# Optimization experiments

Measured on AMD Instinct MI355X. Metric: run time of the kernel, lower is better.

Reference implementation:

```python
import jax, jax.numpy as jnp
import numpy as np

B, L, S, H, E = 2, 2048, 2048, 16, 64


def setup_inputs() -> dict:
    key = jax.random.key(0)
    kq, kk, kv = jax.random.split(key, 3)
    queries = jax.random.normal(kq, (B, L, H, E), dtype=jnp.float32)
    keys = jax.random.normal(kk, (B, S, H, E), dtype=jnp.float32)
    values = jax.random.normal(kv, (B, S, H, E), dtype=jnp.float32)
    attn_mask = jnp.ones((B, 1, L, S), dtype=jnp.float32)  # >0.5 means attend
    return {"queries": queries, "keys": keys, "values": values, "attn_mask": attn_mask}


def reference(queries, keys, values, attn_mask):
    # queries: [B,L,H,E], keys/values: [B,S,H,E], attn_mask broadcastable to [B,H,L,S]
    E_ = queries.shape[-1]
    scale = 1.0 / np.sqrt(E_).astype(np.float32)
    scores = jnp.einsum('blhe,bshe->bhls', queries, keys)  # [B,H,L,S]
    large_negative = jnp.float32(-1e9)
    scores = scores + jnp.where(attn_mask > 0.5, jnp.float32(0.0), large_negative)
    A = jax.nn.softmax(scale * scores, axis=-1)  # dropout p=0.0 -> identity
    V = jnp.einsum('bhls,bshd->bhld', A, values)  # [B,H,L,D]
    return V
```

## Files before the change

### kernel.cpp

```cpp
#include <hip/hip_runtime.h>

typedef float f32x4 __attribute__((ext_vector_type(4)));
typedef short s16x8 __attribute__((ext_vector_type(8)));
typedef int   i32x4 __attribute__((ext_vector_type(4)));
typedef int   i32x2 __attribute__((ext_vector_type(2)));

namespace {
constexpr int B_ = 2, L_ = 2048, S_ = 2048, H_ = 16, E_ = 64;
constexpr int MBLK = 128;
constexpr int NT = 64;
constexpr int NTILES = S_ / NT;
constexpr int KPAD = 72;

#define SCALE2f 0.1803368801111204f
#define MBIAS2f -1.8033688e8f

__device__ __forceinline__ unsigned pk2(float a, float b) {
  unsigned ua = __builtin_bit_cast(unsigned, a) + 0x8000u;
  unsigned ub = __builtin_bit_cast(unsigned, b) + 0x8000u;
  return __builtin_amdgcn_perm(ub, ua, 0x07060302u);
}
__device__ __forceinline__ short f2bs(float x) {
  return (short)((__builtin_bit_cast(unsigned, x) + 0x8000u) >> 16);
}
}

extern "C" __global__ __launch_bounds__(256)
void maskpack_kernel(const float* __restrict__ Mg, unsigned long long* __restrict__ Wb) {
  const int w    = (int)((blockIdx.x * 256 + threadIdx.x) >> 6);
  const int lane = threadIdx.x & 63;
  const float* src = Mg + (size_t)w * 4096 + lane;
  unsigned long long* dst = Wb + (size_t)w * 64;
#pragma unroll 4
  for (int j = 0; j < 64; ++j) {
    const float m = src[j * 64];
    const unsigned long long bits = __ballot(m > 0.5f);
    if (lane == 0) dst[j] = bits;
  }
}

extern "C" __global__ __launch_bounds__(256, 2)
void fattn_kernel(const float* __restrict__ Qg, const float* __restrict__ Kg,
                  const float* __restrict__ Vg, const unsigned long long* __restrict__ Wb,
                  float* __restrict__ Og) {
  __shared__ __align__(16) short Ks[2][NT][KPAD];
  __shared__ __align__(16) short Vt[2][E_][KPAD];
  __shared__ __align__(16) short Ps[4][32][KPAD];

  const int tid  = threadIdx.x;
  const int wv   = tid >> 6;
  const int lane = tid & 63;
  const int qd   = lane >> 4;
  const int cl   = lane & 15;

  const int bid = blockIdx.x;
  const int qb  = bid >> 5;
  const int bh  = bid & 31;
  const int h   = bh & (H_ - 1);
  const int b   = bh >> 4;

  const int l0 = qb * MBLK + wv * 32;

  s16x8 qf[2][2];
#pragma unroll
  for (int mt = 0; mt < 2; ++mt) {
    const float* qp = Qg + ((((size_t)b * L_ + (l0 + mt * 16 + cl)) * H_ + h) << 6);
#pragma unroll
    for (int kb = 0; kb < 2; ++kb) {
      const int e0 = qd * 8 + kb * 32;
      f32x4 x = *(const f32x4*)(qp + e0);
      f32x4 y = *(const f32x4*)(qp + e0 + 4);
      i32x4 w = {(int)pk2(x[0], x[1]), (int)pk2(x[2], x[3]),
                 (int)pk2(y[0], y[1]), (int)pk2(y[2], y[3])};
      qf[mt][kb] = __builtin_bit_cast(s16x8, w);
    }
  }

  const int krow = tid >> 2;
  const int kc0  = (tid & 3) << 4;
  const int vs   = tid & 63;
  const int ve0  = (tid >> 6) << 4;

  const float* kptr = Kg + ((((size_t)b * S_ + krow) * H_ + h) << 6) + kc0;
  const float* vptr = Vg + ((((size_t)b * S_ + vs) * H_ + h) << 6) + ve0;
  const size_t tstep = (size_t)NT * H_ * E_;

  const unsigned long long* wbp[2];
  wbp[0] = Wb + (((size_t)b * L_ + (l0 + cl)) << 5);
  wbp[1] = Wb + (((size_t)b * L_ + (l0 + 16 + cl)) << 5);

  f32x4 kr[4], vr[4];
#pragma unroll
  for (int i = 0; i < 4; ++i) {
    kr[i] = *(const f32x4*)(kptr + i * 4);
    vr[i] = *(const f32x4*)(vptr + i * 4);
  }

  const f32x4 zero4 = {0.f, 0.f, 0.f, 0.f};
  f32x4 acc[2][4];
#pragma unroll
  for (int mt = 0; mt < 2; ++mt)
#pragma unroll
    for (int et = 0; et < 4; ++et) acc[mt][et] = zero4;
  f32x4 rs4[2] = {zero4, zero4};

  {
    i32x4 w0 = {(int)pk2(kr[0][0], kr[0][1]), (int)pk2(kr[0][2], kr[0][3]),
                (int)pk2(kr[1][0], kr[1][1]), (int)pk2(kr[1][2], kr[1][3])};
    i32x4 w1 = {(int)pk2(kr[2][0], kr[2][1]), (int)pk2(kr[2][2], kr[2][3]),
                (int)pk2(kr[3][0], kr[3][1]), (int)pk2(kr[3][2], kr[3][3])};
    *(i32x4*)&Ks[0][krow][kc0]     = w0;
    *(i32x4*)&Ks[0][krow][kc0 + 8] = w1;
#pragma unroll
    for (int j = 0; j < 4; ++j)
#pragma unroll
      for (int c = 0; c < 4; ++c) Vt[0][ve0 + j * 4 + c][vs] = f2bs(vr[j][c]);
  }
#pragma unroll
  for (int i = 0; i < 4; ++i) {
    kr[i] = *(const f32x4*)(kptr + tstep + i * 4);
    vr[i] = *(const f32x4*)(vptr + tstep + i * 4);
  }
  unsigned long long mwcur[2] = {wbp[0][0], wbp[1][0]};

  for (int t = 0; t < NTILES; ++t) {
    const int cb = t & 1;
    __syncthreads();

    unsigned long long mwnext[2];
    if (t + 1 < NTILES) {
      mwnext[0] = wbp[0][t + 1];
      mwnext[1] = wbp[1][t + 1];
    }

    f32x4 sc[4][2];
#pragma unroll
    for (int nt = 0; nt < 4; ++nt) {
      const s16x8 a0 = *(const s16x8*)&Ks[cb][nt * 16 + cl][qd * 8];
      const s16x8 a1 = *(const s16x8*)&Ks[cb][nt * 16 + cl][qd * 8 + 32];
#pragma unroll
      for (int mt = 0; mt < 2; ++mt) {
        f32x4 c = zero4;
        c = __builtin_amdgcn_mfma_f32_16x16x32_bf16(a0, qf[mt][0], c, 0, 0, 0);
        c = __builtin_amdgcn_mfma_f32_16x16x32_bf16(a1, qf[mt][1], c, 0, 0, 0);
        sc[nt][mt] = c;
      }
    }

#pragma unroll
    for (int mt = 0; mt < 2; ++mt) {
      const unsigned lo = (unsigned)mwcur[mt];
      const unsigned hi = (unsigned)(mwcur[mt] >> 32);
#pragma unroll
      for (int nt = 0; nt < 4; ++nt) {
        const unsigned sh = ((nt < 2) ? lo : hi) >> ((nt & 1) * 16 + qd * 4);
        f32x4 p;
#pragma unroll
        for (int r = 0; r < 4; ++r) {
          const float bias = (sh & (1u << r)) ? 0.f : MBIAS2f;
          p[r] = __builtin_amdgcn_exp2f(__builtin_fmaf(sc[nt][mt][r], SCALE2f, bias));
        }
        rs4[mt] += p;
        i32x2 w = {(int)pk2(p[0], p[1]), (int)pk2(p[2], p[3])};
        *(i32x2*)&Ps[wv][mt * 16 + cl][nt * 16 + qd * 4] = w;
      }
    }
    __asm__ volatile("s_waitcnt lgkmcnt(0)" ::: "memory");

#pragma unroll
    for (int kb = 0; kb < 2; ++kb) {
      const s16x8 pb0 = *(const s16x8*)&Ps[wv][cl][kb * 32 + qd * 8];
      const s16x8 pb1 = *(const s16x8*)&Ps[wv][16 + cl][kb * 32 + qd * 8];
#pragma unroll
      for (int et = 0; et < 4; ++et) {
        const s16x8 av = *(const s16x8*)&Vt[cb][et * 16 + cl][kb * 32 + qd * 8];
        acc[0][et] = __builtin_amdgcn_mfma_f32_16x16x32_bf16(av, pb0, acc[0][et], 0, 0, 0);
        acc[1][et] = __builtin_amdgcn_mfma_f32_16x16x32_bf16(av, pb1, acc[1][et], 0, 0, 0);
      }
    }

    if (t + 1 < NTILES) {
      i32x4 w0 = {(int)pk2(kr[0][0], kr[0][1]), (int)pk2(kr[0][2], kr[0][3]),
                  (int)pk2(kr[1][0], kr[1][1]), (int)pk2(kr[1][2], kr[1][3])};
      i32x4 w1 = {(int)pk2(kr[2][0], kr[2][1]), (int)pk2(kr[2][2], kr[2][3]),
                  (int)pk2(kr[3][0], kr[3][1]), (int)pk2(kr[3][2], kr[3][3])};
      *(i32x4*)&Ks[cb ^ 1][krow][kc0]     = w0;
      *(i32x4*)&Ks[cb ^ 1][krow][kc0 + 8] = w1;
#pragma unroll
      for (int j = 0; j < 4; ++j)
#pragma unroll
        for (int c = 0; c < 4; ++c) Vt[cb ^ 1][ve0 + j * 4 + c][vs] = f2bs(vr[j][c]);
    }
    if (t + 2 < NTILES) {
      const float* kp = kptr + (size_t)(t + 2) * tstep;
      const float* vp = vptr + (size_t)(t + 2) * tstep;
#pragma unroll
      for (int i = 0; i < 4; ++i) {
        kr[i] = *(const f32x4*)(kp + i * 4);
        vr[i] = *(const f32x4*)(vp + i * 4);
      }
    }
    if (t + 1 < NTILES) {
      mwcur[0] = mwnext[0];
      mwcur[1] = mwnext[1];
    }
  }

#pragma unroll
  for (int mt = 0; mt < 2; ++mt) {
    float v = rs4[mt][0] + rs4[mt][1] + rs4[mt][2] + rs4[mt][3];
    v += __shfl_xor(v, 16, 64);
    v += __shfl_xor(v, 32, 64);
    const float inv = 1.0f / v;
    const int l = l0 + mt * 16 + cl;
    float* op = Og + ((((size_t)b * H_ + h) * L_ + l) << 6) + qd * 4;
#pragma unroll
    for (int et = 0; et < 4; ++et) {
      f32x4 o = acc[mt][et] * inv;
      *(f32x4*)(op + et * 16) = o;
    }
  }
}

extern "C" void kernel_launch(void* const* d_in, const int* in_sizes, int n_in,
                              void* d_out, int out_size, void* d_ws, size_t ws_size,
                              hipStream_t stream) {
  const float* Q = (const float*)d_in[0];
  const float* K = (const float*)d_in[1];
  const float* V = (const float*)d_in[2];
  const float* M = (const float*)d_in[3];
  float* O = (float*)d_out;
  unsigned long long* Wb = (unsigned long long*)d_ws;

  hipLaunchKernelGGL(maskpack_kernel, dim3(512), dim3(256), 0, stream, M, Wb);
  hipLaunchKernelGGL(fattn_kernel, dim3(B_ * H_ * (L_ / MBLK)), dim3(256), 0, stream,
                     Q, K, V, Wb, O);
}
```

Baseline: 192.3 us.

## Switch to fp16 MFMA, keep P in registers, add all-ones mask fast path

Moves from bf16 to fp16 operands using the packed convert-with-round-toward-zero instruction. The probability tile now stays in registers and feeds 16x16x16 fp16 MFMAs directly, which removes the per-wave shared-memory P round trip and its waitcnt. The V transpose store now writes paired f16x2 values instead of scalar shorts, and a branch skips the mask bias when a mask word is all ones. The mask-pack kernel is reshaped to one wave per row, and the output write layout changes to scalar stores, which may be less coalesced; fp16 also narrows the exponent range of the inputs.

```diff
diff --git a/kernel.cpp b/kernel.cpp
--- a/kernel.cpp
+++ b/kernel.cpp
@@ -1,9 +1,10 @@
 #include <hip/hip_runtime.h>
 
-typedef float f32x4 __attribute__((ext_vector_type(4)));
-typedef short s16x8 __attribute__((ext_vector_type(8)));
-typedef int   i32x4 __attribute__((ext_vector_type(4)));
-typedef int   i32x2 __attribute__((ext_vector_type(2)));
+typedef float    f32x4 __attribute__((ext_vector_type(4)));
+typedef _Float16 f16x2 __attribute__((ext_vector_type(2)));
+typedef _Float16 f16x4 __attribute__((ext_vector_type(4)));
+typedef _Float16 f16x8 __attribute__((ext_vector_type(8)));
+typedef int      i32x4 __attribute__((ext_vector_type(4)));
 
 namespace {
 constexpr int B_ = 2, L_ = 2048, S_ = 2048, H_ = 16, E_ = 64;
@@ -15,26 +16,25 @@
 #define SCALE2f 0.1803368801111204f
 #define MBIAS2f -1.8033688e8f
 
-__device__ __forceinline__ unsigned pk2(float a, float b) {
-  unsigned ua = __builtin_bit_cast(unsigned, a) + 0x8000u;
-  unsigned ub = __builtin_bit_cast(unsigned, b) + 0x8000u;
-  return __builtin_amdgcn_perm(ub, ua, 0x07060302u);
-}
-__device__ __forceinline__ short f2bs(float x) {
-  return (short)((__builtin_bit_cast(unsigned, x) + 0x8000u) >> 16);
-}
+__device__ __forceinline__ f16x2 cvt2(float a, float b) {
+  return __builtin_bit_cast(f16x2, __builtin_amdgcn_cvt_pkrtz(a, b));
+}
+__device__ __forceinline__ int pkh(float a, float b) {
+  return __builtin_bit_cast(int, __builtin_amdgcn_cvt_pkrtz(a, b));
+}
+union H8 { f16x8 v; i32x4 i; };
+union H4 { f16x4 v; f16x2 h[2]; };
 }
 
 extern "C" __global__ __launch_bounds__(256)
 void maskpack_kernel(const float* __restrict__ Mg, unsigned long long* __restrict__ Wb) {
   const int w    = (int)((blockIdx.x * 256 + threadIdx.x) >> 6);
   const int lane = threadIdx.x & 63;
-  const float* src = Mg + (size_t)w * 4096 + lane;
-  unsigned long long* dst = Wb + (size_t)w * 64;
-#pragma unroll 4
-  for (int j = 0; j < 64; ++j) {
-    const float m = src[j * 64];
-    const unsigned long long bits = __ballot(m > 0.5f);
+  const float* src = Mg + (size_t)w * 2048 + lane;
+  unsigned long long* dst = Wb + (size_t)w * 32;
+#pragma unroll 8
+  for (int j = 0; j < 32; ++j) {
+    const unsigned long long bits = __ballot(src[j * 64] > 0.5f);
     if (lane == 0) dst[j] = bits;
   }
 }
@@ -43,9 +43,8 @@
 void fattn_kernel(const float* __restrict__ Qg, const float* __restrict__ Kg,
                   const float* __restrict__ Vg, const unsigned long long* __restrict__ Wb,
                   float* __restrict__ Og) {
-  __shared__ __align__(16) short Ks[2][NT][KPAD];
-  __shared__ __align__(16) short Vt[2][E_][KPAD];
-  __shared__ __align__(16) short Ps[4][32][KPAD];
+  __shared__ __align__(16) _Float16 Ks[2][NT][KPAD];
+  __shared__ __align__(16) _Float16 Vt[2][E_][KPAD];
 
   const int tid  = threadIdx.x;
   const int wv   = tid >> 6;
@@ -61,7 +60,7 @@
 
   const int l0 = qb * MBLK + wv * 32;
 
-  s16x8 qf[2][2];
+  f16x8 qf[2][2];
 #pragma unroll
   for (int mt = 0; mt < 2; ++mt) {
     const float* qp = Qg + ((((size_t)b * L_ + (l0 + mt * 16 + cl)) * H_ + h) << 6);
@@ -70,31 +69,31 @@
       const int e0 = qd * 8 + kb * 32;
       f32x4 x = *(const f32x4*)(qp + e0);
       f32x4 y = *(const f32x4*)(qp + e0 + 4);
-      i32x4 w = {(int)pk2(x[0], x[1]), (int)pk2(x[2], x[3]),
-                 (int)pk2(y[0], y[1]), (int)pk2(y[2], y[3])};
-      qf[mt][kb] = __builtin_bit_cast(s16x8, w);
+      H8 u;
+      u.i = (i32x4){pkh(x[0], x[1]), pkh(x[2], x[3]), pkh(y[0], y[1]), pkh(y[2], y[3])};
+      qf[mt][kb] = u.v;
     }
   }
 
   const int krow = tid >> 2;
   const int kc0  = (tid & 3) << 4;
-  const int vs   = tid & 63;
-  const int ve0  = (tid >> 6) << 4;
-
-  const float* kptr = Kg + ((((size_t)b * S_ + krow) * H_ + h) << 6) + kc0;
-  const float* vptr = Vg + ((((size_t)b * S_ + vs) * H_ + h) << 6) + ve0;
+  const int vcol = tid & 31;
+  const int ve0  = (tid >> 5) << 3;
+
+  const float* kptr  = Kg + ((((size_t)b * S_ + krow) * H_ + h) << 6) + kc0;
+  const float* vptrA = Vg + ((((size_t)b * S_ + 2 * vcol) * H_ + h) << 6) + ve0;
+  const float* vptrB = vptrA + (H_ << 6);
   const size_t tstep = (size_t)NT * H_ * E_;
 
   const unsigned long long* wbp[2];
   wbp[0] = Wb + (((size_t)b * L_ + (l0 + cl)) << 5);
   wbp[1] = Wb + (((size_t)b * L_ + (l0 + 16 + cl)) << 5);
 
-  f32x4 kr[4], vr[4];
-#pragma unroll
-  for (int i = 0; i < 4; ++i) {
-    kr[i] = *(const f32x4*)(kptr + i * 4);
-    vr[i] = *(const f32x4*)(vptr + i * 4);
-  }
+  f32x4 kr[4], va[2], vb[2];
+#pragma unroll
+  for (int i = 0; i < 4; ++i) kr[i] = *(const f32x4*)(kptr + i * 4);
+  va[0] = *(const f32x4*)(vptrA + 0); va[1] = *(const f32x4*)(vptrA + 4);
+  vb[0] = *(const f32x4*)(vptrB + 0); vb[1] = *(const f32x4*)(vptrB + 4);
 
   const f32x4 zero4 = {0.f, 0.f, 0.f, 0.f};
   f32x4 acc[2][4];
@@ -105,105 +104,119 @@
   f32x4 rs4[2] = {zero4, zero4};
 
   {
-    i32x4 w0 = {(int)pk2(kr[0][0], kr[0][1]), (int)pk2(kr[0][2], kr[0][3]),
-                (int)pk2(kr[1][0], kr[1][1]), (int)pk2(kr[1][2], kr[1][3])};
-    i32x4 w1 = {(int)pk2(kr[2][0], kr[2][1]), (int)pk2(kr[2][2], kr[2][3]),
-                (int)pk2(kr[3][0], kr[3][1]), (int)pk2(kr[3][2], kr[3][3])};
+    i32x4 w0 = {pkh(kr[0][0], kr[0][1]), pkh(kr[0][2], kr[0][3]),
+                pkh(kr[1][0], kr[1][1]), pkh(kr[1][2], kr[1][3])};
+    i32x4 w1 = {pkh(kr[2][0], kr[2][1]), pkh(kr[2][2], kr[2][3]),
+                pkh(kr[3][0], kr[3][1]), pkh(kr[3][2], kr[3][3])};
     *(i32x4*)&Ks[0][krow][kc0]     = w0;
     *(i32x4*)&Ks[0][krow][kc0 + 8] = w1;
 #pragma unroll
-    for (int j = 0; j < 4; ++j)
-#pragma unroll
-      for (int c = 0; c < 4; ++c) Vt[0][ve0 + j * 4 + c][vs] = f2bs(vr[j][c]);
-  }
-#pragma unroll
-  for (int i = 0; i < 4; ++i) {
-    kr[i] = *(const f32x4*)(kptr + tstep + i * 4);
-    vr[i] = *(const f32x4*)(vptr + tstep + i * 4);
-  }
+    for (int j = 0; j < 4; ++j) {
+      *(f16x2*)&Vt[0][ve0 + j][2 * vcol]     = cvt2(va[0][j], vb[0][j]);
+      *(f16x2*)&Vt[0][ve0 + 4 + j][2 * vcol] = cvt2(va[1][j], vb[1][j]);
+    }
+  }
+#pragma unroll
+  for (int i = 0; i < 4; ++i) kr[i] = *(const f32x4*)(kptr + tstep + i * 4);
+  va[0] = *(const f32x4*)(vptrA + tstep + 0); va[1] = *(const f32x4*)(vptrA + tstep + 4);
+  vb[0] = *(const f32x4*)(vptrB + tstep + 0); vb[1] = *(const f32x4*)(vptrB + tstep + 4);
+
   unsigned long long mwcur[2] = {wbp[0][0], wbp[1][0]};
 
   for (int t = 0; t < NTILES; ++t) {
     const int cb = t & 1;
     __syncthreads();
 
-    unsigned long long mwnext[2];
-    if (t + 1 < NTILES) {
-      mwnext[0] = wbp[0][t + 1];
-      mwnext[1] = wbp[1][t + 1];
-    }
+    unsigned long long mwnext0 = 0, mwnext1 = 0;
+    if (t + 1 < NTILES) { mwnext0 = wbp[0][t + 1]; mwnext1 = wbp[1][t + 1]; }
 
     f32x4 sc[4][2];
 #pragma unroll
     for (int nt = 0; nt < 4; ++nt) {
-      const s16x8 a0 = *(const s16x8*)&Ks[cb][nt * 16 + cl][qd * 8];
-      const s16x8 a1 = *(const s16x8*)&Ks[cb][nt * 16 + cl][qd * 8 + 32];
+      const f16x8 a0 = *(const f16x8*)&Ks[cb][nt * 16 + cl][qd * 8];
+      const f16x8 a1 = *(const f16x8*)&Ks[cb][nt * 16 + cl][qd * 8 + 32];
 #pragma unroll
       for (int mt = 0; mt < 2; ++mt) {
         f32x4 c = zero4;
-        c = __builtin_amdgcn_mfma_f32_16x16x32_bf16(a0, qf[mt][0], c, 0, 0, 0);
-        c = __builtin_amdgcn_mfma_f32_16x16x32_bf16(a1, qf[mt][1], c, 0, 0, 0);
+        c = __builtin_amdgcn_mfma_f32_16x16x32_f16(a0, qf[mt][0], c, 0, 0, 0);
+        c = __builtin_amdgcn_mfma_f32_16x16x32_f16(a1, qf[mt][1], c, 0, 0, 0);
         sc[nt][mt] = c;
       }
     }
 
-#pragma unroll
-    for (int mt = 0; mt < 2; ++mt) {
-      const unsigned lo = (unsigned)mwcur[mt];
-      const unsigned hi = (unsigned)(mwcur[mt] >> 32);
-#pragma unroll
-      for (int nt = 0; nt < 4; ++nt) {
-        const unsigned sh = ((nt < 2) ? lo : hi) >> ((nt & 1) * 16 + qd * 4);
-        f32x4 p;
-#pragma unroll
-        for (int r = 0; r < 4; ++r) {
-          const float bias = (sh & (1u << r)) ? 0.f : MBIAS2f;
-          p[r] = __builtin_amdgcn_exp2f(__builtin_fmaf(sc[nt][mt][r], SCALE2f, bias));
-        }
-        rs4[mt] += p;
-        i32x2 w = {(int)pk2(p[0], p[1]), (int)pk2(p[2], p[3])};
-        *(i32x2*)&Ps[wv][mt * 16 + cl][nt * 16 + qd * 4] = w;
-      }
-    }
-    __asm__ volatile("s_waitcnt lgkmcnt(0)" ::: "memory");
-
-#pragma unroll
-    for (int kb = 0; kb < 2; ++kb) {
-      const s16x8 pb0 = *(const s16x8*)&Ps[wv][cl][kb * 32 + qd * 8];
-      const s16x8 pb1 = *(const s16x8*)&Ps[wv][16 + cl][kb * 32 + qd * 8];
-#pragma unroll
-      for (int et = 0; et < 4; ++et) {
-        const s16x8 av = *(const s16x8*)&Vt[cb][et * 16 + cl][kb * 32 + qd * 8];
-        acc[0][et] = __builtin_amdgcn_mfma_f32_16x16x32_bf16(av, pb0, acc[0][et], 0, 0, 0);
-        acc[1][et] = __builtin_amdgcn_mfma_f32_16x16x32_bf16(av, pb1, acc[1][et], 0, 0, 0);
-      }
-    }
-
     if (t + 1 < NTILES) {
-      i32x4 w0 = {(int)pk2(kr[0][0], kr[0][1]), (int)pk2(kr[0][2], kr[0][3]),
-                  (int)pk2(kr[1][0], kr[1][1]), (int)pk2(kr[1][2], kr[1][3])};
-      i32x4 w1 = {(int)pk2(kr[2][0], kr[2][1]), (int)pk2(kr[2][2], kr[2][3]),
-                  (int)pk2(kr[3][0], kr[3][1]), (int)pk2(kr[3][2], kr[3][3])};
+      i32x4 w0 = {pkh(kr[0][0], kr[0][1]), pkh(kr[0][2], kr[0][3]),
+                  pkh(kr[1][0], kr[1][1]), pkh(kr[1][2], kr[1][3])};
+      i32x4 w1 = {pkh(kr[2][0], kr[2][1]), pkh(kr[2][2], kr[2][3]),
+                  pkh(kr[3][0], kr[3][1]), pkh(kr[3][2], kr[3][3])};
       *(i32x4*)&Ks[cb ^ 1][krow][kc0]     = w0;
       *(i32x4*)&Ks[cb ^ 1][krow][kc0 + 8] = w1;
 #pragma unroll
-      for (int j = 0; j < 4; ++j)
-#pragma unroll
-        for (int c = 0; c < 4; ++c) Vt[cb ^ 1][ve0 + j * 4 + c][vs] = f2bs(vr[j][c]);
-    }
+      for (int j = 0; j < 4; ++j) {
+        *(f16x2*)&Vt[cb ^ 1][ve0 + j][2 * vcol]     = cvt2(va[0][j], vb[0][j]);
+        *(f16x2*)&Vt[cb ^ 1][ve0 + 4 + j][2 * vcol] = cvt2(va[1][j], vb[1][j]);
+      }
+    }
+
+    f16x4 pa[2][4];
+    if (mwcur[0] == ~0ull && mwcur[1] == ~0ull) {
+#pragma unroll
+      for (int mt = 0; mt < 2; ++mt)
+#pragma unroll
+        for (int nt = 0; nt < 4; ++nt) {
+          f32x4 p;
+#pragma unroll
+          for (int r = 0; r < 4; ++r)
+            p[r] = __builtin_amdgcn_exp2f(sc[nt][mt][r] * SCALE2f);
+          rs4[mt] += p;
+          H4 u;
+          u.h[0] = cvt2(p[0], p[1]);
+          u.h[1] = cvt2(p[2], p[3]);
+          pa[mt][nt] = u.v;
+        }
+    } else {
+#pragma unroll
+      for (int mt = 0; mt < 2; ++mt) {
+        const unsigned lo = (unsigned)mwcur[mt];
+        const unsigned hi = (unsigned)(mwcur[mt] >> 32);
+#pragma unroll
+        for (int nt = 0; nt < 4; ++nt) {
+          const unsigned sh = ((nt < 2) ? lo : hi) >> ((nt & 1) * 16 + qd * 4);
+          f32x4 p;
+#pragma unroll
+          for (int r = 0; r < 4; ++r) {
+            const float bias = (sh & (1u << r)) ? 0.f : MBIAS2f;
+            p[r] = __builtin_amdgcn_exp2f(__builtin_fmaf(sc[nt][mt][r], SCALE2f, bias));
+          }
+          rs4[mt] += p;
+          H4 u;
+          u.h[0] = cvt2(p[0], p[1]);
+          u.h[1] = cvt2(p[2], p[3]);
+          pa[mt][nt] = u.v;
+        }
+      }
+    }
+
+#pragma unroll
+    for (int nt = 0; nt < 4; ++nt)
+#pragma unroll
+      for (int et = 0; et < 4; ++et) {
+        const f16x4 bv = *(const f16x4*)&Vt[cb][et * 16 + cl][nt * 16 + qd * 4];
+        acc[0][et] = __builtin_amdgcn_mfma_f32_16x16x16f16(pa[0][nt], bv, acc[0][et], 0, 0, 0);
+        acc[1][et] = __builtin_amdgcn_mfma_f32_16x16x16f16(pa[1][nt], bv, acc[1][et], 0, 0, 0);
+      }
+
     if (t + 2 < NTILES) {
       const float* kp = kptr + (size_t)(t + 2) * tstep;
-      const float* vp = vptr + (size_t)(t + 2) * tstep;
-#pragma unroll
-      for (int i = 0; i < 4; ++i) {
-        kr[i] = *(const f32x4*)(kp + i * 4);
-        vr[i] = *(const f32x4*)(vp + i * 4);
-      }
-    }
-    if (t + 1 < NTILES) {
-      mwcur[0] = mwnext[0];
-      mwcur[1] = mwnext[1];
-    }
+      const float* vpA = vptrA + (size_t)(t + 2) * tstep;
+      const float* vpB = vptrB + (size_t)(t + 2) * tstep;
+#pragma unroll
+      for (int i = 0; i < 4; ++i) kr[i] = *(const f32x4*)(kp + i * 4);
+      va[0] = *(const f32x4*)(vpA + 0); va[1] = *(const f32x4*)(vpA + 4);
+      vb[0] = *(const f32x4*)(vpB + 0); vb[1] = *(const f32x4*)(vpB + 4);
+    }
+    mwcur[0] = mwnext0;
+    mwcur[1] = mwnext1;
   }
 
 #pragma unroll
@@ -211,13 +224,13 @@
     float v = rs4[mt][0] + rs4[mt][1] + rs4[mt][2] + rs4[mt][3];
     v += __shfl_xor(v, 16, 64);
     v += __shfl_xor(v, 32, 64);
-    const float inv = 1.0f / v;
-    const int l = l0 + mt * 16 + cl;
-    float* op = Og + ((((size_t)b * H_ + h) * L_ + l) << 6) + qd * 4;
-#pragma unroll
-    for (int et = 0; et < 4; ++et) {
-      f32x4 o = acc[mt][et] * inv;
-      *(f32x4*)(op + et * 16) = o;
+#pragma unroll
+    for (int r = 0; r < 4; ++r) {
+      const float invq = 1.0f / __shfl(v, qd * 4 + r, 64);
+      const int l = l0 + mt * 16 + qd * 4 + r;
+      float* op = Og + ((((size_t)b * H_ + h) * L_ + l) << 6) + cl;
+#pragma unroll
+      for (int et = 0; et < 4; ++et) op[et * 16] = acc[mt][et][r] * invq;
     }
   }
 }
@@ -232,7 +245,7 @@
   float* O = (float*)d_out;
   unsigned long long* Wb = (unsigned long long*)d_ws;
 
-  hipLaunchKernelGGL(maskpack_kernel, dim3(512), dim3(256), 0, stream, M, Wb);
+  hipLaunchKernelGGL(maskpack_kernel, dim3(B_ * L_ / 4), dim3(256), 0, stream, M, Wb);
   hipLaunchKernelGGL(fattn_kernel, dim3(B_ * H_ * (L_ / MBLK)), dim3(256), 0, stream,
                      Q, K, V, Wb, O);
 }
```

Result: faster. 178.2 us (-7.3%).
